# Optimization experiments

Measured on AMD Instinct MI355X. Metric: run time of the kernel, lower is better.

## Reference

```python
import jax, jax.numpy as jnp
import numpy as np

TOTAL = 16777216  # total nodes across all graphs
N = 65536         # number of graphs (len(v_count))
K = 16            # k_pool


def setup_inputs() -> dict:
    key = jax.random.key(0)
    k1, k2 = jax.random.split(key)
    Y = jax.random.normal(k1, (TOTAL, 1), dtype=jnp.float32)
    W = jnp.ones((K,), dtype=jnp.float32)  # initializer Ones, as in build()
    e_map = jnp.sort(jax.random.randint(k2, (TOTAL,), 0, N, dtype=jnp.int32))
    v_count = jnp.ones((N,), dtype=jnp.int32)  # only its length is used
    return {"Y": Y, "W": W, "e_map": e_map, "v_count": v_count}


def reference(Y, W, e_map, v_count):
    # Faithful SortPooling forward. Instead of materializing the padded
    # [N, max_seg_len] -inf tensor, we do k_pool fused segment-max passes:
    # each pass extracts the current per-segment max and masks out exactly
    # one occurrence (the first, by index) -- identical to tf.math.top_k on
    # the -inf-padded ragged-to-dense tensor (ties yield duplicate values,
    # matching top_k semantics).
    n = v_count.shape[0]
    k = W.shape[0]  # static k_pool; segments here are much larger than k
    y = jnp.squeeze(Y, axis=-1)  # [TOTAL]
    total = y.shape[0]
    idxs = jnp.arange(total, dtype=jnp.int32)
    neg_inf = jnp.float32(-jnp.inf)

    y_work = y
    tops = []
    for _ in range(k):
        m = jax.ops.segment_max(y_work, e_map, num_segments=n)  # [N]
        tops.append(m)
        is_max = y_work == m[e_map]
        # first index attaining the max in each segment (total == sentinel)
        first = jax.ops.segment_min(jnp.where(is_max, idxs, total),
                                    e_map, num_segments=n)  # [N]
        # OOB indices (exhausted/empty segments) are dropped by scatter
        y_work = y_work.at[first].set(neg_inf)

    Y_top = jnp.stack(tops, axis=-1)        # [N, k] sorted descending
    Wn = jax.nn.softmax(W)                  # [k]
    Y_w = jnp.where(jnp.isinf(Y_top), jnp.float32(0.0), Y_top) * Wn
    return jnp.sum(Y_w, axis=-1)            # [N]
```

## Files before the change

kernel.cpp:

```cpp
#include <hip/hip_runtime.h>
#include <math.h>

#define KPOOL 16
#define SPLIT 8

typedef float f32x4 __attribute__((ext_vector_type(4)));

__device__ __forceinline__ void ce(float& x, float& y) {
  float hi = fmaxf(x, y), lo = fminf(x, y);
  x = hi;
  y = lo;
}

__device__ __forceinline__ void sort8(float (&v)[8]) {
  ce(v[0], v[1]); ce(v[2], v[3]); ce(v[4], v[5]); ce(v[6], v[7]);
  ce(v[0], v[2]); ce(v[1], v[3]); ce(v[4], v[6]); ce(v[5], v[7]);
  ce(v[1], v[2]); ce(v[5], v[6]);
  ce(v[0], v[4]); ce(v[1], v[5]); ce(v[2], v[6]); ce(v[3], v[7]);
  ce(v[2], v[4]); ce(v[3], v[5]);
  ce(v[1], v[2]); ce(v[3], v[4]); ce(v[5], v[6]);
}

__device__ __forceinline__ void merge8into16(float (&t)[KPOOL], const float (&b)[8]) {
#pragma unroll
  for (int i = 8; i < 16; ++i) t[i] = fmaxf(t[i], b[15 - i]);
#pragma unroll
  for (int s = 8; s >= 1; s >>= 1) {
#pragma unroll
    for (int i = 0; i < 16; ++i)
      if ((i & s) == 0) ce(t[i], t[i + s]);
  }
}

__device__ __forceinline__ void merge_partner(float (&t)[KPOOL], int dist) {
  float c[KPOOL];
#pragma unroll
  for (int i = 0; i < KPOOL; ++i) {
    float o = __shfl_xor(t[KPOOL - 1 - i], dist);
    c[i] = fmaxf(t[i], o);
  }
#pragma unroll
  for (int s = 8; s >= 1; s >>= 1) {
#pragma unroll
    for (int i = 0; i < KPOOL; ++i)
      if ((i & s) == 0) ce(c[i], c[i + s]);
  }
#pragma unroll
  for (int i = 0; i < KPOOL; ++i) t[i] = c[i];
}

__device__ __forceinline__ int lb_range(const int* __restrict__ a, int lo,
                                        int hi, int key) {
  while (lo < hi) {
    int mid = (lo + hi) >> 1;
    if (a[mid] < key) lo = mid + 1;
    else hi = mid;
  }
  return lo;
}

__global__ __launch_bounds__(256)
void boundary_kernel(const int* __restrict__ emap, int total, int n,
                     int* __restrict__ starts, float* __restrict__ wn_out,
                     const float* __restrict__ W) {
  const int g = blockIdx.x * 256 + threadIdx.x;
  if (g == 0) {
    float w[KPOOL], m = -INFINITY, s = 0.0f;
#pragma unroll
    for (int k = 0; k < KPOOL; ++k) { w[k] = W[k]; m = fmaxf(m, w[k]); }
#pragma unroll
    for (int k = 0; k < KPOOL; ++k) { w[k] = expf(w[k] - m); s += w[k]; }
#pragma unroll
    for (int k = 0; k < KPOOL; ++k) wn_out[k] = w[k] / s;
  }
  if (g > n) return;
  if (g == 0) { starts[0] = 0; return; }
  if (g >= n) { starts[n] = total; return; }

  const int key = g;
  const int W0 = 32768;
  if (total < W0) { starts[g] = lb_range(emap, 0, total, key); return; }

  long long E = (long long)key * total / n;
  int wlo = (int)(E - W0 / 2);
  if (wlo < 0) wlo = 0;
  if (wlo > total - W0) wlo = total - W0;

  int p[7];
#pragma unroll
  for (int k = 0; k < 7; ++k) p[k] = emap[wlo + (k + 1) * 4096];
  const int vlo = (wlo > 0) ? emap[wlo - 1] : (key - 1) - key;
  const int vhi = emap[wlo + W0 - 1];
  const bool ok = (vlo < key) && ((wlo + W0 == total) || (vhi >= key));
  if (!ok) { starts[g] = lb_range(emap, 0, total, key); return; }

  int lo = wlo;
  int c = 0;
#pragma unroll
  for (int k = 0; k < 7; ++k) c += (p[k] < key) ? 1 : 0;
  lo += c * 4096;

#pragma unroll
  for (int w8 = 512; w8 >= 1; w8 >>= 3) {
#pragma unroll
    for (int k = 0; k < 7; ++k) p[k] = emap[lo + (k + 1) * w8];
    c = 0;
#pragma unroll
    for (int k = 0; k < 7; ++k) c += (p[k] < key) ? 1 : 0;
    lo += c * w8;
  }
  starts[g] = (emap[lo] < key) ? lo + 1 : lo;
}

__global__ __launch_bounds__(256, 4)
void sortpool_main(const float* __restrict__ Y,
                   const int* __restrict__ starts,
                   const float* __restrict__ Wn,
                   float* __restrict__ out, int total, int n) {
  const int tid = blockIdx.x * 256 + threadIdx.x;
  const int g = tid >> 3;
  const int q = tid & 7;
  if (g >= n) return;

  const int s0 = starts[g];
  const int s1 = starts[g + 1];
  const unsigned len = (unsigned)(s1 - s0);

  const int B0 = s0 >> 3;
  const int B1 = (s1 + 7) >> 3;
  const int BLAST = (total >> 3) - 1;

  float t[KPOOL];
#pragma unroll
  for (int i = 0; i < KPOOL; ++i) t[i] = -INFINITY;

  int b = B0 + q;
  {
    const int a0 = b <= BLAST ? b : BLAST;
    const f32x4* p = reinterpret_cast<const f32x4*>(Y + (a0 << 3));
    f32x4 c0 = p[0];
    f32x4 c1 = p[1];
#pragma unroll 1
    while (b < B1) {
      const int bn = b + SPLIT;
      const int an = bn < B1 ? bn : b;
      const f32x4* pn = reinterpret_cast<const f32x4*>(Y + (an << 3));
      f32x4 n0 = pn[0];
      f32x4 n1 = pn[1];
      const int base = b << 3;
      float v[8] = {c0[0], c0[1], c0[2], c0[3], c1[0], c1[1], c1[2], c1[3]};
#pragma unroll
      for (int jj = 0; jj < 8; ++jj) {
        if ((unsigned)(base + jj - s0) >= len) v[jj] = -INFINITY;
      }
      sort8(v);
      merge8into16(t, v);
      c0 = n0;
      c1 = n1;
      b = bn;
    }
  }

  merge_partner(t, 1);
  merge_partner(t, 2);
  merge_partner(t, 4);

  float res = 0.0f;
#pragma unroll
  for (int k = 0; k < KPOOL; ++k) {
    float tv = t[k];
    res += (tv > -INFINITY) ? tv * Wn[k] : 0.0f;
  }

  if (q == 0) out[g] = res;
}

__global__ __launch_bounds__(256, 4)
void sortpool_main_nows(const float* __restrict__ Y, const float* __restrict__ W,
                        const int* __restrict__ emap, float* __restrict__ out,
                        int total, int n) {
  const int tid = blockIdx.x * 256 + threadIdx.x;
  const int g = tid >> 3;
  const int q = tid & 7;
  if (g >= n) return;
  const int s0 = lb_range(emap, 0, total, g);
  const int s1 = lb_range(emap, 0, total, g + 1);
  const unsigned len = (unsigned)(s1 - s0);
  const int B0 = s0 >> 3;
  const int B1 = (s1 + 7) >> 3;
  const int BLAST = (total >> 3) - 1;
  float t[KPOOL];
#pragma unroll
  for (int i = 0; i < KPOOL; ++i) t[i] = -INFINITY;
  int b = B0 + q;
  const int a0 = b <= BLAST ? b : BLAST;
  const f32x4* p = reinterpret_cast<const f32x4*>(Y + (a0 << 3));
  f32x4 c0 = p[0], c1 = p[1];
#pragma unroll 1
  while (b < B1) {
    const int bn = b + SPLIT;
    const int an = bn < B1 ? bn : b;
    const f32x4* pn = reinterpret_cast<const f32x4*>(Y + (an << 3));
    f32x4 n0 = pn[0], n1 = pn[1];
    const int base = b << 3;
    float v[8] = {c0[0], c0[1], c0[2], c0[3], c1[0], c1[1], c1[2], c1[3]};
#pragma unroll
    for (int jj = 0; jj < 8; ++jj)
      if ((unsigned)(base + jj - s0) >= len) v[jj] = -INFINITY;
    sort8(v);
    merge8into16(t, v);
    c0 = n0; c1 = n1; b = bn;
  }
  merge_partner(t, 1);
  merge_partner(t, 2);
  merge_partner(t, 4);
  float wv[KPOOL], m = -INFINITY, s = 0.0f;
#pragma unroll
  for (int k = 0; k < KPOOL; ++k) { wv[k] = W[k]; m = fmaxf(m, wv[k]); }
#pragma unroll
  for (int k = 0; k < KPOOL; ++k) { wv[k] = expf(wv[k] - m); s += wv[k]; }
  const float inv = 1.0f / s;
  float res = 0.0f;
#pragma unroll
  for (int k = 0; k < KPOOL; ++k) {
    float tv = t[k];
    res += (tv > -INFINITY) ? tv * (wv[k] * inv) : 0.0f;
  }
  if (q == 0) out[g] = res;
}

extern "C" void kernel_launch(void* const* d_in, const int* in_sizes, int n_in,
                              void* d_out, int out_size, void* d_ws, size_t ws_size,
                              hipStream_t stream) {
  const float* Y = (const float*)d_in[0];
  const float* W = (const float*)d_in[1];
  const int* emap = (const int*)d_in[2];
  const int total = in_sizes[0];
  const int n = in_sizes[3];
  float* out = (float*)d_out;

  int* starts = (int*)d_ws;
  float* wn_buf = (float*)((char*)d_ws + (size_t)(n + 1) * sizeof(int));
  const bool use_ws =
      (ws_size >= (size_t)(n + 1) * sizeof(int) + KPOOL * sizeof(float));

  long long threads = (long long)n * SPLIT;
  int blocks = (int)((threads + 255) / 256);

  if (use_ws) {
    int nb = (n + 1 + 255) / 256;
    boundary_kernel<<<nb, 256, 0, stream>>>(emap, total, n, starts, wn_buf, W);
    sortpool_main<<<blocks, 256, 0, stream>>>(Y, starts, wn_buf, out, total, n);
  } else {
    sortpool_main_nows<<<blocks, 256, 0, stream>>>(Y, W, emap, out, total, n);
  }
}
```

Baseline: 37.50 us.

## Use two threads per segment with two-deep load prefetch

Each segment is now handled by 2 threads instead of 8, so there is more serial work per thread and only one cross-lane merge step instead of three. The load pipeline goes two iterations deep, and the per-element masking is skipped for chunks that lie entirely inside the segment. This cuts shuffle/merge overhead and redundant tail work at the cost of fewer threads in flight and longer per-thread loops. Average segments hold about 256 elements, so each thread now processes about 16 chunks.

```diff
diff --git a/kernel.cpp b/kernel.cpp
--- a/kernel.cpp
+++ b/kernel.cpp
@@ -2,7 +2,7 @@
 #include <math.h>
 
 #define KPOOL 16
-#define SPLIT 8
+#define SPLIT 2
 
 typedef float f32x4 __attribute__((ext_vector_type(4)));
 
@@ -89,7 +89,7 @@
   int p[7];
 #pragma unroll
   for (int k = 0; k < 7; ++k) p[k] = emap[wlo + (k + 1) * 4096];
-  const int vlo = (wlo > 0) ? emap[wlo - 1] : (key - 1) - key;
+  const int vlo = (wlo > 0) ? emap[wlo - 1] : key - 1 - key;
   const int vhi = emap[wlo + W0 - 1];
   const bool ok = (vlo < key) && ((wlo + W0 == total) || (vhi >= key));
   if (!ok) { starts[g] = lb_range(emap, 0, total, key); return; }
@@ -118,13 +118,12 @@
                    const float* __restrict__ Wn,
                    float* __restrict__ out, int total, int n) {
   const int tid = blockIdx.x * 256 + threadIdx.x;
-  const int g = tid >> 3;
-  const int q = tid & 7;
+  const int g = tid >> 1;
+  const int q = tid & 1;
   if (g >= n) return;
 
   const int s0 = starts[g];
   const int s1 = starts[g + 1];
-  const unsigned len = (unsigned)(s1 - s0);
 
   const int B0 = s0 >> 3;
   const int B1 = (s1 + 7) >> 3;
@@ -135,35 +134,39 @@
   for (int i = 0; i < KPOOL; ++i) t[i] = -INFINITY;
 
   int b = B0 + q;
+  f32x4 c0, c1, m0, m1;
   {
     const int a0 = b <= BLAST ? b : BLAST;
     const f32x4* p = reinterpret_cast<const f32x4*>(Y + (a0 << 3));
-    f32x4 c0 = p[0];
-    f32x4 c1 = p[1];
+    c0 = p[0]; c1 = p[1];
+    const int b1 = b + SPLIT;
+    const int a1 = b1 <= BLAST ? b1 : BLAST;
+    const f32x4* p1 = reinterpret_cast<const f32x4*>(Y + (a1 << 3));
+    m0 = p1[0]; m1 = p1[1];
+  }
 #pragma unroll 1
-    while (b < B1) {
-      const int bn = b + SPLIT;
-      const int an = bn < B1 ? bn : b;
-      const f32x4* pn = reinterpret_cast<const f32x4*>(Y + (an << 3));
-      f32x4 n0 = pn[0];
-      f32x4 n1 = pn[1];
-      const int base = b << 3;
-      float v[8] = {c0[0], c0[1], c0[2], c0[3], c1[0], c1[1], c1[2], c1[3]};
+  while (b < B1) {
+    const int b2 = b + 2 * SPLIT;
+    const int a2 = b2 <= BLAST ? b2 : BLAST;
+    const f32x4* p2 = reinterpret_cast<const f32x4*>(Y + (a2 << 3));
+    f32x4 g0 = p2[0];
+    f32x4 g1 = p2[1];
+    const int base = b << 3;
+    float v[8] = {c0[0], c0[1], c0[2], c0[3], c1[0], c1[1], c1[2], c1[3]};
+    if (base < s0 || base + 8 > s1) {
 #pragma unroll
       for (int jj = 0; jj < 8; ++jj) {
-        if ((unsigned)(base + jj - s0) >= len) v[jj] = -INFINITY;
+        int idx = base + jj;
+        if (idx < s0 || idx >= s1) v[jj] = -INFINITY;
       }
-      sort8(v);
-      merge8into16(t, v);
-      c0 = n0;
-      c1 = n1;
-      b = bn;
     }
+    sort8(v);
+    merge8into16(t, v);
+    c0 = m0; c1 = m1; m0 = g0; m1 = g1;
+    b += SPLIT;
   }
 
   merge_partner(t, 1);
-  merge_partner(t, 2);
-  merge_partner(t, 4);
 
   float res = 0.0f;
 #pragma unroll
@@ -180,12 +183,11 @@
                         const int* __restrict__ emap, float* __restrict__ out,
                         int total, int n) {
   const int tid = blockIdx.x * 256 + threadIdx.x;
-  const int g = tid >> 3;
-  const int q = tid & 7;
+  const int g = tid >> 1;
+  const int q = tid & 1;
   if (g >= n) return;
   const int s0 = lb_range(emap, 0, total, g);
   const int s1 = lb_range(emap, 0, total, g + 1);
-  const unsigned len = (unsigned)(s1 - s0);
   const int B0 = s0 >> 3;
   const int B1 = (s1 + 7) >> 3;
   const int BLAST = (total >> 3) - 1;
@@ -193,27 +195,38 @@
 #pragma unroll
   for (int i = 0; i < KPOOL; ++i) t[i] = -INFINITY;
   int b = B0 + q;
-  const int a0 = b <= BLAST ? b : BLAST;
-  const f32x4* p = reinterpret_cast<const f32x4*>(Y + (a0 << 3));
-  f32x4 c0 = p[0], c1 = p[1];
+  f32x4 c0, c1, m0, m1;
+  {
+    const int a0 = b <= BLAST ? b : BLAST;
+    const f32x4* p = reinterpret_cast<const f32x4*>(Y + (a0 << 3));
+    c0 = p[0]; c1 = p[1];
+    const int b1 = b + SPLIT;
+    const int a1 = b1 <= BLAST ? b1 : BLAST;
+    const f32x4* p1 = reinterpret_cast<const f32x4*>(Y + (a1 << 3));
+    m0 = p1[0]; m1 = p1[1];
+  }
 #pragma unroll 1
   while (b < B1) {
-    const int bn = b + SPLIT;
-    const int an = bn < B1 ? bn : b;
-    const f32x4* pn = reinterpret_cast<const f32x4*>(Y + (an << 3));
-    f32x4 n0 = pn[0], n1 = pn[1];
+    const int b2 = b + 2 * SPLIT;
+    const int a2 = b2 <= BLAST ? b2 : BLAST;
+    const f32x4* p2 = reinterpret_cast<const f32x4*>(Y + (a2 << 3));
+    f32x4 g0 = p2[0];
+    f32x4 g1 = p2[1];
     const int base = b << 3;
     float v[8] = {c0[0], c0[1], c0[2], c0[3], c1[0], c1[1], c1[2], c1[3]};
-#pragma unroll
-    for (int jj = 0; jj < 8; ++jj)
-      if ((unsigned)(base + jj - s0) >= len) v[jj] = -INFINITY;
+    if (base < s0 || base + 8 > s1) {
+#pragma unroll
+      for (int jj = 0; jj < 8; ++jj) {
+        int idx = base + jj;
+        if (idx < s0 || idx >= s1) v[jj] = -INFINITY;
+      }
+    }
     sort8(v);
     merge8into16(t, v);
-    c0 = n0; c1 = n1; b = bn;
+    c0 = m0; c1 = m1; m0 = g0; m1 = g1;
+    b += SPLIT;
   }
   merge_partner(t, 1);
-  merge_partner(t, 2);
-  merge_partner(t, 4);
   float wv[KPOOL], m = -INFINITY, s = 0.0f;
 #pragma unroll
   for (int k = 0; k < KPOOL; ++k) { wv[k] = W[k]; m = fmaxf(m, wv[k]); }
```

Result: faster. 33.53 us (-10.6%).

## Use two threads per segment with four-deep load pipeline in scan

Applied to the files above, without the earlier changes.

Reduces threads per segment from eight to two, so each thread scans more blocks and only one cross-lane merge is needed instead of three. The scan loop is unrolled four ways and keeps four 8-element loads in flight, and the boundary masking is skipped for blocks fully inside the segment. Block size drops to 128. This trades thread-level parallelism for memory-level parallelism per thread and less merge overhead, at the cost of more registers and fewer waves overall.

```diff
diff --git a/kernel.cpp b/kernel.cpp
--- a/kernel.cpp
+++ b/kernel.cpp
@@ -2,7 +2,7 @@
 #include <math.h>
 
 #define KPOOL 16
-#define SPLIT 8
+#define SPLIT 2
 
 typedef float f32x4 __attribute__((ext_vector_type(4)));
 
@@ -89,7 +89,7 @@
   int p[7];
 #pragma unroll
   for (int k = 0; k < 7; ++k) p[k] = emap[wlo + (k + 1) * 4096];
-  const int vlo = (wlo > 0) ? emap[wlo - 1] : (key - 1) - key;
+  const int vlo = (wlo > 0) ? emap[wlo - 1] : key - 1 - key;
   const int vhi = emap[wlo + W0 - 1];
   const bool ok = (vlo < key) && ((wlo + W0 == total) || (vhi >= key));
   if (!ok) { starts[g] = lb_range(emap, 0, total, key); return; }
@@ -112,58 +112,72 @@
   starts[g] = (emap[lo] < key) ? lo + 1 : lo;
 }
 
-__global__ __launch_bounds__(256, 4)
+#define LOADB(R0, R1, bb)                                              \
+  {                                                                    \
+    const int cb_ = (bb) <= BLAST ? (bb) : BLAST;                      \
+    const f32x4* p_ = reinterpret_cast<const f32x4*>(Y + (cb_ << 3));  \
+    R0 = p_[0];                                                        \
+    R1 = p_[1];                                                        \
+  }
+
+#define STEPP(R0, R1, bb, nb)                                          \
+  {                                                                    \
+    float v[8] = {R0[0], R0[1], R0[2], R0[3], R1[0], R1[1], R1[2], R1[3]}; \
+    LOADB(R0, R1, nb);                                                 \
+    const int base_ = (bb) << 3;                                       \
+    if (base_ < s0 || base_ + 8 > s1) {                                \
+      _Pragma("unroll") for (int jj = 0; jj < 8; ++jj) {               \
+        int idx_ = base_ + jj;                                         \
+        if (idx_ < s0 || idx_ >= s1) v[jj] = -INFINITY;                \
+      }                                                                \
+    }                                                                  \
+    sort8(v);                                                          \
+    merge8into16(t, v);                                                \
+  }
+
+__device__ __forceinline__ void scan_segment(const float* __restrict__ Y,
+                                             int s0, int s1, int q, int total,
+                                             float (&t)[KPOOL]) {
+  const int B0 = s0 >> 3;
+  const int B1 = (s1 + 7) >> 3;
+  const int BLAST = (total >> 3) - 1;
+
+  int b = B0 + q;
+  f32x4 A0, A1, Bb0, Bb1, C0, C1, D0, D1;
+  LOADB(A0, A1, b);
+  LOADB(Bb0, Bb1, b + SPLIT);
+  LOADB(C0, C1, b + 2 * SPLIT);
+  LOADB(D0, D1, b + 3 * SPLIT);
+#pragma unroll 1
+  while (b < B1) {
+    STEPP(A0, A1, b, b + 4 * SPLIT);
+    STEPP(Bb0, Bb1, b + SPLIT, b + 5 * SPLIT);
+    STEPP(C0, C1, b + 2 * SPLIT, b + 6 * SPLIT);
+    STEPP(D0, D1, b + 3 * SPLIT, b + 7 * SPLIT);
+    b += 4 * SPLIT;
+  }
+}
+
+__global__ __launch_bounds__(128, 4)
 void sortpool_main(const float* __restrict__ Y,
                    const int* __restrict__ starts,
                    const float* __restrict__ Wn,
                    float* __restrict__ out, int total, int n) {
-  const int tid = blockIdx.x * 256 + threadIdx.x;
-  const int g = tid >> 3;
-  const int q = tid & 7;
+  const int tid = blockIdx.x * 128 + threadIdx.x;
+  const int g = tid >> 1;
+  const int q = tid & 1;
   if (g >= n) return;
 
   const int s0 = starts[g];
   const int s1 = starts[g + 1];
-  const unsigned len = (unsigned)(s1 - s0);
-
-  const int B0 = s0 >> 3;
-  const int B1 = (s1 + 7) >> 3;
-  const int BLAST = (total >> 3) - 1;
 
   float t[KPOOL];
 #pragma unroll
   for (int i = 0; i < KPOOL; ++i) t[i] = -INFINITY;
 
-  int b = B0 + q;
-  {
-    const int a0 = b <= BLAST ? b : BLAST;
-    const f32x4* p = reinterpret_cast<const f32x4*>(Y + (a0 << 3));
-    f32x4 c0 = p[0];
-    f32x4 c1 = p[1];
-#pragma unroll 1
-    while (b < B1) {
-      const int bn = b + SPLIT;
-      const int an = bn < B1 ? bn : b;
-      const f32x4* pn = reinterpret_cast<const f32x4*>(Y + (an << 3));
-      f32x4 n0 = pn[0];
-      f32x4 n1 = pn[1];
-      const int base = b << 3;
-      float v[8] = {c0[0], c0[1], c0[2], c0[3], c1[0], c1[1], c1[2], c1[3]};
-#pragma unroll
-      for (int jj = 0; jj < 8; ++jj) {
-        if ((unsigned)(base + jj - s0) >= len) v[jj] = -INFINITY;
-      }
-      sort8(v);
-      merge8into16(t, v);
-      c0 = n0;
-      c1 = n1;
-      b = bn;
-    }
-  }
+  scan_segment(Y, s0, s1, q, total, t);
 
   merge_partner(t, 1);
-  merge_partner(t, 2);
-  merge_partner(t, 4);
 
   float res = 0.0f;
 #pragma unroll
@@ -175,45 +189,21 @@
   if (q == 0) out[g] = res;
 }
 
-__global__ __launch_bounds__(256, 4)
+__global__ __launch_bounds__(128, 4)
 void sortpool_main_nows(const float* __restrict__ Y, const float* __restrict__ W,
                         const int* __restrict__ emap, float* __restrict__ out,
                         int total, int n) {
-  const int tid = blockIdx.x * 256 + threadIdx.x;
-  const int g = tid >> 3;
-  const int q = tid & 7;
+  const int tid = blockIdx.x * 128 + threadIdx.x;
+  const int g = tid >> 1;
+  const int q = tid & 1;
   if (g >= n) return;
   const int s0 = lb_range(emap, 0, total, g);
   const int s1 = lb_range(emap, 0, total, g + 1);
-  const unsigned len = (unsigned)(s1 - s0);
-  const int B0 = s0 >> 3;
-  const int B1 = (s1 + 7) >> 3;
-  const int BLAST = (total >> 3) - 1;
   float t[KPOOL];
 #pragma unroll
   for (int i = 0; i < KPOOL; ++i) t[i] = -INFINITY;
-  int b = B0 + q;
-  const int a0 = b <= BLAST ? b : BLAST;
-  const f32x4* p = reinterpret_cast<const f32x4*>(Y + (a0 << 3));
-  f32x4 c0 = p[0], c1 = p[1];
-#pragma unroll 1
-  while (b < B1) {
-    const int bn = b + SPLIT;
-    const int an = bn < B1 ? bn : b;
-    const f32x4* pn = reinterpret_cast<const f32x4*>(Y + (an << 3));
-    f32x4 n0 = pn[0], n1 = pn[1];
-    const int base = b << 3;
-    float v[8] = {c0[0], c0[1], c0[2], c0[3], c1[0], c1[1], c1[2], c1[3]};
-#pragma unroll
-    for (int jj = 0; jj < 8; ++jj)
-      if ((unsigned)(base + jj - s0) >= len) v[jj] = -INFINITY;
-    sort8(v);
-    merge8into16(t, v);
-    c0 = n0; c1 = n1; b = bn;
-  }
+  scan_segment(Y, s0, s1, q, total, t);
   merge_partner(t, 1);
-  merge_partner(t, 2);
-  merge_partner(t, 4);
   float wv[KPOOL], m = -INFINITY, s = 0.0f;
 #pragma unroll
   for (int k = 0; k < KPOOL; ++k) { wv[k] = W[k]; m = fmaxf(m, wv[k]); }
@@ -245,13 +235,13 @@
       (ws_size >= (size_t)(n + 1) * sizeof(int) + KPOOL * sizeof(float));
 
   long long threads = (long long)n * SPLIT;
-  int blocks = (int)((threads + 255) / 256);
+  int blocks = (int)((threads + 127) / 128);
 
   if (use_ws) {
     int nb = (n + 1 + 255) / 256;
     boundary_kernel<<<nb, 256, 0, stream>>>(emap, total, n, starts, wn_buf, W);
-    sortpool_main<<<blocks, 256, 0, stream>>>(Y, starts, wn_buf, out, total, n);
+    sortpool_main<<<blocks, 128, 0, stream>>>(Y, starts, wn_buf, out, total, n);
   } else {
-    sortpool_main_nows<<<blocks, 256, 0, stream>>>(Y, W, emap, out, total, n);
-  }
-}
+    sortpool_main_nows<<<blocks, 128, 0, stream>>>(Y, W, emap, out, total, n);
+  }
+}
```

Measured after the change: 36.29 us. 1.03x faster.

## Stage each block's contiguous Y range into LDS via async global_load_lds

Applied to the files above, without the earlier changes.

The main kernel now assigns 32 graphs per block and first copies the block's whole contiguous Y span (up to 9216 floats) into shared memory with the global-to-LDS load builtin, then each 8-thread group reads its segment from LDS, falling back to global loads past the cap. This replaces the per-thread software-prefetched strided global loads with fully coalesced bulk staging. The cost is an LDS footprint of about 36 KB per block, which limits occupancy, plus a barrier that serialises load and compute inside each block. The no-workspace path also drops its prefetch pipeline.

```diff
diff --git a/kernel.cpp b/kernel.cpp
--- a/kernel.cpp
+++ b/kernel.cpp
@@ -3,6 +3,8 @@
 
 #define KPOOL 16
 #define SPLIT 8
+#define GPB 32
+#define CAP 9216
 
 typedef float f32x4 __attribute__((ext_vector_type(4)));
 
@@ -89,7 +91,7 @@
   int p[7];
 #pragma unroll
   for (int k = 0; k < 7; ++k) p[k] = emap[wlo + (k + 1) * 4096];
-  const int vlo = (wlo > 0) ? emap[wlo - 1] : (key - 1) - key;
+  const int vlo = (wlo > 0) ? emap[wlo - 1] : key - 1 - key;
   const int vhi = emap[wlo + W0 - 1];
   const bool ok = (vlo < key) && ((wlo + W0 == total) || (vhi >= key));
   if (!ok) { starts[g] = lb_range(emap, 0, total, key); return; }
@@ -113,66 +115,82 @@
 }
 
 __global__ __launch_bounds__(256, 4)
-void sortpool_main(const float* __restrict__ Y,
-                   const int* __restrict__ starts,
-                   const float* __restrict__ Wn,
-                   float* __restrict__ out, int total, int n) {
-  const int tid = blockIdx.x * 256 + threadIdx.x;
-  const int g = tid >> 3;
+void sortpool_lds(const float* __restrict__ Y,
+                  const int* __restrict__ starts,
+                  const float* __restrict__ Wn,
+                  float* __restrict__ out, int total, int n) {
+  __shared__ float buf[CAP];
+  const int tid = threadIdx.x;
+  const int g0 = blockIdx.x * GPB;
+  if (g0 >= n) return;
+  const int gend = (g0 + GPB < n) ? g0 + GPB : n;
+  const int g = g0 + (tid >> 3);
   const int q = tid & 7;
-  if (g >= n) return;
-
-  const int s0 = starts[g];
-  const int s1 = starts[g + 1];
-  const unsigned len = (unsigned)(s1 - s0);
-
-  const int B0 = s0 >> 3;
-  const int B1 = (s1 + 7) >> 3;
-  const int BLAST = (total >> 3) - 1;
-
-  float t[KPOOL];
-#pragma unroll
-  for (int i = 0; i < KPOOL; ++i) t[i] = -INFINITY;
-
-  int b = B0 + q;
-  {
-    const int a0 = b <= BLAST ? b : BLAST;
-    const f32x4* p = reinterpret_cast<const f32x4*>(Y + (a0 << 3));
-    f32x4 c0 = p[0];
-    f32x4 c1 = p[1];
+
+  const int base = starts[g0] & ~7;
+  const int end = starts[gend];
+  int staged = (end - base + 3) & ~3;
+  const int lim = total - base;
+  if (staged > CAP) staged = CAP;
+  if (staged > lim) staged = lim;
+
+  for (int off = tid * 4; off < staged; off += 1024) {
+    __builtin_amdgcn_global_load_lds(
+        (const __attribute__((address_space(1))) void*)(Y + base + off),
+        (__attribute__((address_space(3))) void*)(buf + off), 16, 0, 0);
+  }
+  __syncthreads();
+
+  if (g < gend) {
+    const int s0 = starts[g];
+    const int s1 = starts[g + 1];
+
+    float t[KPOOL];
+#pragma unroll
+    for (int i = 0; i < KPOOL; ++i) t[i] = -INFINITY;
+
+    const int B0 = s0 >> 3;
+    const int B1 = (s1 + 7) >> 3;
 #pragma unroll 1
-    while (b < B1) {
-      const int bn = b + SPLIT;
-      const int an = bn < B1 ? bn : b;
-      const f32x4* pn = reinterpret_cast<const f32x4*>(Y + (an << 3));
-      f32x4 n0 = pn[0];
-      f32x4 n1 = pn[1];
-      const int base = b << 3;
-      float v[8] = {c0[0], c0[1], c0[2], c0[3], c1[0], c1[1], c1[2], c1[3]};
-#pragma unroll
-      for (int jj = 0; jj < 8; ++jj) {
-        if ((unsigned)(base + jj - s0) >= len) v[jj] = -INFINITY;
+    for (int b = B0 + q; b < B1; b += SPLIT) {
+      const int off = (b << 3) - base;
+      float v[8];
+      if (off + 8 <= staged) {
+        const f32x4* p = reinterpret_cast<const f32x4*>(buf + off);
+        const f32x4 a = p[0], c = p[1];
+        v[0] = a[0]; v[1] = a[1]; v[2] = a[2]; v[3] = a[3];
+        v[4] = c[0]; v[5] = c[1]; v[6] = c[2]; v[7] = c[3];
+      } else {
+#pragma unroll
+        for (int jj = 0; jj < 8; ++jj) {
+          const int idx = (b << 3) + jj;
+          v[jj] = (idx < total) ? Y[idx] : -INFINITY;
+        }
+      }
+      const int bbase = b << 3;
+      if (bbase < s0 || bbase + 8 > s1) {
+#pragma unroll
+        for (int jj = 0; jj < 8; ++jj) {
+          const int idx = bbase + jj;
+          if (idx < s0 || idx >= s1) v[jj] = -INFINITY;
+        }
       }
       sort8(v);
       merge8into16(t, v);
-      c0 = n0;
-      c1 = n1;
-      b = bn;
     }
-  }
-
-  merge_partner(t, 1);
-  merge_partner(t, 2);
-  merge_partner(t, 4);
-
-  float res = 0.0f;
-#pragma unroll
-  for (int k = 0; k < KPOOL; ++k) {
-    float tv = t[k];
-    res += (tv > -INFINITY) ? tv * Wn[k] : 0.0f;
-  }
-
-  if (q == 0) out[g] = res;
+
+    merge_partner(t, 1);
+    merge_partner(t, 2);
+    merge_partner(t, 4);
+
+    float res = 0.0f;
+#pragma unroll
+    for (int k = 0; k < KPOOL; ++k) {
+      const float tv = t[k];
+      res += (tv > -INFINITY) ? tv * Wn[k] : 0.0f;
+    }
+    if (q == 0) out[g] = res;
+  }
 }
 
 __global__ __launch_bounds__(256, 4)
@@ -185,31 +203,21 @@
   if (g >= n) return;
   const int s0 = lb_range(emap, 0, total, g);
   const int s1 = lb_range(emap, 0, total, g + 1);
-  const unsigned len = (unsigned)(s1 - s0);
+  float t[KPOOL];
+#pragma unroll
+  for (int i = 0; i < KPOOL; ++i) t[i] = -INFINITY;
   const int B0 = s0 >> 3;
   const int B1 = (s1 + 7) >> 3;
-  const int BLAST = (total >> 3) - 1;
-  float t[KPOOL];
-#pragma unroll
-  for (int i = 0; i < KPOOL; ++i) t[i] = -INFINITY;
-  int b = B0 + q;
-  const int a0 = b <= BLAST ? b : BLAST;
-  const f32x4* p = reinterpret_cast<const f32x4*>(Y + (a0 << 3));
-  f32x4 c0 = p[0], c1 = p[1];
 #pragma unroll 1
-  while (b < B1) {
-    const int bn = b + SPLIT;
-    const int an = bn < B1 ? bn : b;
-    const f32x4* pn = reinterpret_cast<const f32x4*>(Y + (an << 3));
-    f32x4 n0 = pn[0], n1 = pn[1];
-    const int base = b << 3;
-    float v[8] = {c0[0], c0[1], c0[2], c0[3], c1[0], c1[1], c1[2], c1[3]};
-#pragma unroll
-    for (int jj = 0; jj < 8; ++jj)
-      if ((unsigned)(base + jj - s0) >= len) v[jj] = -INFINITY;
+  for (int b = B0 + q; b < B1; b += SPLIT) {
+    float v[8];
+#pragma unroll
+    for (int jj = 0; jj < 8; ++jj) {
+      const int idx = (b << 3) + jj;
+      v[jj] = (idx < total && idx >= s0 && idx < s1) ? Y[idx] : -INFINITY;
+    }
     sort8(v);
     merge8into16(t, v);
-    c0 = n0; c1 = n1; b = bn;
   }
   merge_partner(t, 1);
   merge_partner(t, 2);
@@ -223,7 +231,7 @@
   float res = 0.0f;
 #pragma unroll
   for (int k = 0; k < KPOOL; ++k) {
-    float tv = t[k];
+    const float tv = t[k];
     res += (tv > -INFINITY) ? tv * (wv[k] * inv) : 0.0f;
   }
   if (q == 0) out[g] = res;
@@ -244,14 +252,14 @@
   const bool use_ws =
       (ws_size >= (size_t)(n + 1) * sizeof(int) + KPOOL * sizeof(float));
 
-  long long threads = (long long)n * SPLIT;
-  int blocks = (int)((threads + 255) / 256);
-
   if (use_ws) {
-    int nb = (n + 1 + 255) / 256;
+    const int nb = (n + 1 + 255) / 256;
     boundary_kernel<<<nb, 256, 0, stream>>>(emap, total, n, starts, wn_buf, W);
-    sortpool_main<<<blocks, 256, 0, stream>>>(Y, starts, wn_buf, out, total, n);
+    const int blocks = (n + GPB - 1) / GPB;
+    sortpool_lds<<<blocks, 256, 0, stream>>>(Y, starts, wn_buf, out, total, n);
   } else {
+    long long threads = (long long)n * SPLIT;
+    const int blocks = (int)((threads + 255) / 256);
     sortpool_main_nows<<<blocks, 256, 0, stream>>>(Y, W, emap, out, total, n);
   }
 }
```

Result: slower. 41.89 us (+11.7%).
